# Performance work log

Hardware: AMD Instinct MI355X
Metric: run time of the kernel (lower is better)

## Reference

```python
import jax, jax.numpy as jnp
import numpy as np

B, S, D, H, VOCAB = 4, 2048, 1024, 2048, 32000
E, K, M = 8, 2, 64  # num_experts, top_k, moe_hidden_dim


def gif_forward(x, W, b, decay=0.9, thr=1.0, slope=4.0):
    # GIF neuron layer: linear synaptic current, leaky membrane integration over
    # the sequence dim, surrogate sigmoid spikes with soft reset.
    cur = jnp.einsum('bsd,dh->bsh', x, W) + b  # [B,S,Dout]
    v0 = jnp.zeros((cur.shape[0], cur.shape[2]), cur.dtype)

    def step(v, c):
        v = decay * v + c
        s = jax.nn.sigmoid(slope * (v - thr))
        return v - s * thr, s

    _, spikes = jax.lax.scan(step, v0, jnp.swapaxes(cur, 0, 1))
    return jnp.swapaxes(spikes, 0, 1)  # [B,S,Dout]


def layer_norm(x, g, b, eps=1e-5):
    mu = jnp.mean(x, -1, keepdims=True)
    var = jnp.var(x, -1, keepdims=True)
    return (x - mu) * jax.lax.rsqrt(var + eps) * g + b


def setup_inputs() -> dict:
    key = jax.random.key(0)
    ks = jax.random.split(key, 12)

    def w(k, shape, fan_in):
        return jax.random.normal(k, shape, jnp.float32) / np.sqrt(fan_in).astype(np.float32)

    return {
        'inputs_embeds': jax.random.normal(ks[0], (B, S, D), jnp.float32),
        'input_ids': jax.random.randint(ks[1], (B, S), 0, VOCAB),
        'prosody_table': 0.1 * jax.random.normal(ks[2], (VOCAB,), jnp.float32),
        'enc_W': w(ks[3], (D, H), D), 'enc_b': jnp.zeros((H,), jnp.float32),
        's2c_W': w(ks[4], (H, M), H), 's2c_b': jnp.zeros((M,), jnp.float32),
        'r_W1': w(ks[5], (M, 64), M), 'r_b1': jnp.zeros((64,), jnp.float32),
        'r_W2': w(ks[6], (64, E), 64), 'r_b2': jnp.zeros((E,), jnp.float32),
        'e_W1': w(ks[7], (E, M, H // 2), M), 'e_b1': jnp.zeros((E, H // 2), jnp.float32),
        'e_W2': w(ks[8], (E, H // 2, M), H // 2), 'e_b2': jnp.zeros((E, M), jnp.float32),
        'c2s_W': w(ks[9], (M, H), M), 'c2s_b': jnp.zeros((H,), jnp.float32),
        'dec_W': w(ks[10], (H, D), H), 'dec_b': jnp.zeros((D,), jnp.float32),
        'ln_g': jnp.ones((D,), jnp.float32), 'ln_b': jnp.zeros((D,), jnp.float32),
    }


def reference(inputs_embeds, input_ids, prosody_table, enc_W, enc_b, s2c_W, s2c_b,
              r_W1, r_b1, r_W2, r_b2, e_W1, e_b1, e_W2, e_b2, c2s_W, c2s_b,
              dec_W, dec_b, ln_g, ln_b):
    b, s, d = inputs_embeds.shape
    # Prosody attention bridge: per-token scalar gain from token ids.
    gains = 1.0 + jnp.tanh(prosody_table[input_ids])  # [B,S]
    x = inputs_embeds * gains[..., None]
    spikes = gif_forward(x, enc_W, enc_b)  # [B,S,H]
    # Spike-to-continuous (rate encoding over the singleton time dim) -> [N,M]
    cont = spikes.reshape(b * s, -1) @ s2c_W + s2c_b
    # Liquid MoE router, logits modulated by flattened attention gains.
    logits = (jnp.tanh(cont @ r_W1 + r_b1) @ r_W2 + r_b2) * gains.reshape(-1, 1)
    probs = jax.nn.softmax(logits, axis=-1)  # [N,E]
    topw, topi = jax.lax.top_k(probs, K)
    topw = topw / jnp.sum(topw, axis=-1, keepdims=True)
    # combine[n,e] = sum_k topw[n,k] * [topi[n,k]==e]  (masked-accumulation weights)
    combine = jnp.sum(topw[..., None] * jax.nn.one_hot(topi, E, dtype=probs.dtype), axis=1)
    # Dense-for-all-experts, faithful to the original masked loop.
    h = jax.nn.relu(jnp.einsum('nm,emh->enh', cont, e_W1) + e_b1[:, None, :])  # [E,N,H/2]
    ex_out = jnp.einsum('enh,ehm->enm', h, e_W2) + e_b2[:, None, :]  # [E,N,M]
    moe = jnp.einsum('enm,ne->nm', ex_out, combine)  # [N,M]
    # Continuous-to-spike poisson bridge: T identical rate copies; mean over the
    # copy dim (view(B,S,-1,H).mean(dim=2)) collapses back to the rate itself.
    rates = jax.nn.sigmoid(moe @ c2s_W + c2s_b)  # [N,H]
    spikes_avg = rates.reshape(b, s, -1) * gains[..., None]
    decoded = gif_forward(spikes_avg, dec_W, dec_b)  # [B,S,D]
    return layer_norm(decoded, ln_g, ln_b)
```

## Files before the change

### kernel.cpp

```cpp
#include <hip/hip_runtime.h>
#include <math.h>

#define B_ 4
#define S_ 2048
#define D_ 1024
#define H_ 2048
#define N_TOK 8192
#define HALO 256
#define VOCAB_ 32000

typedef short bf16x8 __attribute__((ext_vector_type(8)));
typedef float f32x4 __attribute__((ext_vector_type(4)));

__device__ __forceinline__ float sigf(float x) {
  return 1.0f / (1.0f + __expf(-x));
}
__device__ __forceinline__ float bf2f(unsigned short u) {
  union { unsigned int i; float f; } x; x.i = ((unsigned int)u) << 16; return x.f;
}
__device__ __forceinline__ unsigned short f2bf(float f) {
  union { float f; unsigned int i; } x; x.f = f;
  unsigned int r = x.i + 0x7fffu + ((x.i >> 16) & 1u);
  return (unsigned short)(r >> 16);
}

__global__ __launch_bounds__(256) void k_gains(const int* __restrict__ ids,
    const float* __restrict__ table, float* __restrict__ gains) {
  int i = blockIdx.x*256 + threadIdx.x;
  int id = ids[i];
  id = id < 0 ? 0 : (id >= VOCAB_ ? VOCAB_-1 : id);
  gains[i] = 1.0f + tanhf(table[id]);
}

__global__ __launch_bounds__(256) void k_genc(
    const float* __restrict__ A, int lda,
    const float* __restrict__ W, int ldw, int c0,
    const float* __restrict__ bias,
    const float* __restrict__ gains,
    float* __restrict__ C, int ldc,
    int K, int mode)
{
  __shared__ float As2[16][132];
  __shared__ float Bs[16][128];
  const int tid = threadIdx.x;
  const int tx = tid & 15;
  const int ty = tid >> 4;
  const int bm = blockIdx.y * 128;
  const int bn = blockIdx.x * 128;

  double acc[8][8];
  float part[8][8];
  #pragma unroll
  for (int i = 0; i < 8; ++i)
    #pragma unroll
    for (int j = 0; j < 8; ++j) { acc[i][j] = 0.0; part[i][j] = 0.f; }

  const int e = tid * 8;
  const int ar = e >> 4, ak = e & 15;
  const int bk = e >> 7, bc = e & 127;

  for (int k0 = 0; k0 < K; k0 += 16) {
    {
      const float* pa = A + (size_t)(bm + ar)*lda + k0 + ak;
      float4 v0 = *(const float4*)pa;
      float4 v1 = *(const float4*)(pa + 4);
      As2[ak+0][ar] = v0.x; As2[ak+1][ar] = v0.y;
      As2[ak+2][ar] = v0.z; As2[ak+3][ar] = v0.w;
      As2[ak+4][ar] = v1.x; As2[ak+5][ar] = v1.y;
      As2[ak+6][ar] = v1.z; As2[ak+7][ar] = v1.w;
    }
    {
      const float* pw = W + (size_t)(k0 + bk)*ldw + c0 + bn + bc;
      *(float4*)&Bs[bk][bc]   = *(const float4*)pw;
      *(float4*)&Bs[bk][bc+4] = *(const float4*)(pw + 4);
    }
    __syncthreads();
    #pragma unroll
    for (int kk = 0; kk < 16; ++kk) {
      float a8[8], b8[8];
      *(float4*)&a8[0] = *(const float4*)&As2[kk][ty*8];
      *(float4*)&a8[4] = *(const float4*)&As2[kk][ty*8+4];
      *(float4*)&b8[0] = *(const float4*)&Bs[kk][tx*8];
      *(float4*)&b8[4] = *(const float4*)&Bs[kk][tx*8+4];
      #pragma unroll
      for (int i = 0; i < 8; ++i)
        #pragma unroll
        for (int j = 0; j < 8; ++j)
          part[i][j] += a8[i]*b8[j];
    }
    __syncthreads();
    #pragma unroll
    for (int i = 0; i < 8; ++i)
      #pragma unroll
      for (int j = 0; j < 8; ++j) { acc[i][j] += (double)part[i][j]; part[i][j] = 0.f; }
  }

  #pragma unroll
  for (int i = 0; i < 8; ++i) {
    const int row = bm + ty*8 + i;
    const double g = (mode >= 2) ? (double)gains[row] : 0.0;
    #pragma unroll
    for (int j = 0; j < 8; ++j) {
      const int col = bn + tx*8 + j;
      const size_t idx = (size_t)row*ldc + col;
      if (mode == 0)      C[idx] = (float)acc[i][j];
      else if (mode == 1) C[idx] += (float)acc[i][j];
      else if (mode == 2) C[idx] = (float)(g*((double)C[idx] + acc[i][j]) + (double)bias[c0+col]);
      else                C[idx] = (float)(g*acc[i][j] + (double)bias[c0+col]);
    }
  }
}

__global__ __launch_bounds__(256) void k_splitT(const float* __restrict__ in,
    unsigned short* __restrict__ outh, unsigned short* __restrict__ outl) {
  __shared__ unsigned short th[32][33];
  __shared__ unsigned short tl[32][33];
  int c0 = blockIdx.x*32, r0 = blockIdx.y*32;
  int tx = threadIdx.x & 31, ty = threadIdx.x >> 5;
  #pragma unroll
  for (int i = 0; i < 32; i += 8) {
    float x = in[(size_t)(r0+ty+i)*H_ + (c0+tx)];
    unsigned short h = f2bf(x);
    th[ty+i][tx] = h;
    tl[ty+i][tx] = f2bf(x - bf2f(h));
  }
  __syncthreads();
  #pragma unroll
  for (int i = 0; i < 32; i += 8) {
    outh[(size_t)(c0+ty+i)*D_ + (r0+tx)] = th[tx][ty+i];
    outl[(size_t)(c0+ty+i)*D_ + (r0+tx)] = tl[tx][ty+i];
  }
}

__global__ __launch_bounds__(256) void k_tsplit(const float* __restrict__ in,
    unsigned short* __restrict__ oh, unsigned short* __restrict__ ol,
    int R, int C) {
  __shared__ unsigned short th[32][33];
  __shared__ unsigned short tl[32][33];
  const size_t mat = (size_t)R*C;
  in += (size_t)blockIdx.z * mat;
  oh += (size_t)blockIdx.z * mat;
  ol += (size_t)blockIdx.z * mat;
  int c0 = blockIdx.x*32, r0 = blockIdx.y*32;
  int tx = threadIdx.x & 31, ty = threadIdx.x >> 5;
  #pragma unroll
  for (int i = 0; i < 32; i += 8) {
    float x = in[(size_t)(r0+ty+i)*C + (c0+tx)];
    unsigned short h = f2bf(x);
    th[ty+i][tx] = h;
    tl[ty+i][tx] = f2bf(x - bf2f(h));
  }
  __syncthreads();
  #pragma unroll
  for (int i = 0; i < 32; i += 8) {
    oh[(size_t)(c0+ty+i)*R + (r0+tx)] = th[tx][ty+i];
    ol[(size_t)(c0+ty+i)*R + (r0+tx)] = tl[tx][ty+i];
  }
}

__global__ __launch_bounds__(256) void k_asplit(const float* __restrict__ in,
    unsigned short* __restrict__ oh, unsigned short* __restrict__ ol) {
  const size_t i = ((size_t)blockIdx.x*256 + threadIdx.x) * 8;
  float4 v0 = *(const float4*)(in + i);
  float4 v1 = *(const float4*)(in + i + 4);
  float xs[8] = {v0.x, v0.y, v0.z, v0.w, v1.x, v1.y, v1.z, v1.w};
  unsigned int hp[4], lp[4];
  #pragma unroll
  for (int t = 0; t < 4; ++t) {
    unsigned short h0 = f2bf(xs[2*t]);
    unsigned short h1 = f2bf(xs[2*t+1]);
    unsigned short l0 = f2bf(xs[2*t]   - bf2f(h0));
    unsigned short l1 = f2bf(xs[2*t+1] - bf2f(h1));
    hp[t] = (unsigned)h0 | ((unsigned)h1 << 16);
    lp[t] = (unsigned)l0 | ((unsigned)l1 << 16);
  }
  *(uint4*)(oh + i) = make_uint4(hp[0], hp[1], hp[2], hp[3]);
  *(uint4*)(ol + i) = make_uint4(lp[0], lp[1], lp[2], lp[3]);
}

__global__ __launch_bounds__(256) void k_egemm(
    const float* __restrict__ A,
    const unsigned short* __restrict__ Bh,
    const unsigned short* __restrict__ Bl,
    const float* __restrict__ bias,
    const float* __restrict__ gains,
    float* __restrict__ C)
{
  __shared__ __align__(16) unsigned short Ahs[128*40];
  __shared__ __align__(16) unsigned short Als[128*40];
  __shared__ __align__(16) unsigned short Bhs[128*40];
  __shared__ __align__(16) unsigned short Bls[128*40];
  const int tid  = threadIdx.x;
  const int lane = tid & 63;
  const int wave = tid >> 6;
  const int wm = (wave >> 1) * 64;
  const int wn = (wave & 1) * 64;
  const int bm = blockIdx.y * 128;
  const int bn = blockIdx.x * 128;
  const int fml = lane & 15;
  const int q  = lane >> 4;
  const int r0a  = tid >> 2;
  const int sseg = tid & 3;

  f32x4 acc[4][4] = {};

  for (int k0 = 0; k0 < 1024; k0 += 32) {
    #pragma unroll
    for (int half = 0; half < 2; ++half) {
      int r = r0a + half*64;
      const float* pa = A + (size_t)(bm + r)*1024 + k0 + sseg*8;
      float4 v0 = *(const float4*)pa;
      float4 v1 = *(const float4*)(pa + 4);
      float xs[8] = {v0.x, v0.y, v0.z, v0.w, v1.x, v1.y, v1.z, v1.w};
      unsigned int hp[4], lp[4];
      #pragma unroll
      for (int t = 0; t < 4; ++t) {
        unsigned short h0 = f2bf(xs[2*t]);
        unsigned short h1 = f2bf(xs[2*t+1]);
        unsigned short l0 = f2bf(xs[2*t]   - bf2f(h0));
        unsigned short l1 = f2bf(xs[2*t+1] - bf2f(h1));
        hp[t] = (unsigned)h0 | ((unsigned)h1 << 16);
        lp[t] = (unsigned)l0 | ((unsigned)l1 << 16);
      }
      *(uint4*)(&Ahs[r*40 + sseg*8]) = make_uint4(hp[0], hp[1], hp[2], hp[3]);
      *(uint4*)(&Als[r*40 + sseg*8]) = make_uint4(lp[0], lp[1], lp[2], lp[3]);
      *(uint4*)(&Bhs[r*40 + sseg*8]) = *(const uint4*)(Bh + (size_t)(bn + r)*1024 + k0 + sseg*8);
      *(uint4*)(&Bls[r*40 + sseg*8]) = *(const uint4*)(Bl + (size_t)(bn + r)*1024 + k0 + sseg*8);
    }
    __syncthreads();
    bf16x8 afh[4], afl[4], bfh[4], bfl[4];
    #pragma unroll
    for (int i = 0; i < 4; ++i) {
      afh[i] = *(const bf16x8*)(&Ahs[(wm + i*16 + fml)*40 + q*8]);
      afl[i] = *(const bf16x8*)(&Als[(wm + i*16 + fml)*40 + q*8]);
    }
    #pragma unroll
    for (int j = 0; j < 4; ++j) {
      bfh[j] = *(const bf16x8*)(&Bhs[(wn + j*16 + fml)*40 + q*8]);
      bfl[j] = *(const bf16x8*)(&Bls[(wn + j*16 + fml)*40 + q*8]);
    }
    #pragma unroll
    for (int i = 0; i < 4; ++i)
      #pragma unroll
      for (int j = 0; j < 4; ++j) {
        acc[i][j] = __builtin_amdgcn_mfma_f32_16x16x32_bf16(afl[i], bfh[j], acc[i][j], 0, 0, 0);
        acc[i][j] = __builtin_amdgcn_mfma_f32_16x16x32_bf16(afh[i], bfl[j], acc[i][j], 0, 0, 0);
        acc[i][j] = __builtin_amdgcn_mfma_f32_16x16x32_bf16(afh[i], bfh[j], acc[i][j], 0, 0, 0);
      }
    __syncthreads();
  }
  #pragma unroll
  for (int i = 0; i < 4; ++i) {
    #pragma unroll
    for (int j = 0; j < 4; ++j) {
      int col = bn + wn + j*16 + fml;
      float bv = bias[col];
      #pragma unroll
      for (int r = 0; r < 4; ++r) {
        int row = bm + wm + i*16 + q*4 + r;
        C[(size_t)row*D_ + col] = gains[row]*acc[i][j][r] + bv;
      }
    }
  }
}

__global__ __launch_bounds__(256) void k_egemm3(
    const unsigned short* __restrict__ Ah, const unsigned short* __restrict__ Al,
    const unsigned short* __restrict__ Bh, const unsigned short* __restrict__ Bl,
    const float* __restrict__ bias,
    const float* __restrict__ gains,
    float* __restrict__ C)
{
  __shared__ __align__(16) unsigned short Ahs[128*40];
  __shared__ __align__(16) unsigned short Als[128*40];
  __shared__ __align__(16) unsigned short Bhs[128*40];
  __shared__ __align__(16) unsigned short Bls[128*40];
  const int tid  = threadIdx.x;
  const int lane = tid & 63;
  const int wave = tid >> 6;
  const int wm = (wave >> 1) * 64;
  const int wn = (wave & 1) * 64;
  const int flat = blockIdx.y * 8 + blockIdx.x;
  const int swz  = (flat & 7) * 64 + (flat >> 3);
  const int bn = (swz & 7) * 128;
  const int bm = (swz >> 3) * 128;
  const int fml = lane & 15;
  const int q  = lane >> 4;
  const int r0a  = tid >> 2;
  const int sseg = tid & 3;

  f32x4 acc[4][4] = {};

  for (int k0 = 0; k0 < 1024; k0 += 32) {
    #pragma unroll
    for (int half = 0; half < 2; ++half) {
      int r = r0a + half*64;
      *(uint4*)(&Ahs[r*40 + sseg*8]) = *(const uint4*)(Ah + (size_t)(bm + r)*1024 + k0 + sseg*8);
      *(uint4*)(&Als[r*40 + sseg*8]) = *(const uint4*)(Al + (size_t)(bm + r)*1024 + k0 + sseg*8);
      *(uint4*)(&Bhs[r*40 + sseg*8]) = *(const uint4*)(Bh + (size_t)(bn + r)*1024 + k0 + sseg*8);
      *(uint4*)(&Bls[r*40 + sseg*8]) = *(const uint4*)(Bl + (size_t)(bn + r)*1024 + k0 + sseg*8);
    }
    __syncthreads();
    bf16x8 afh[4], afl[4], bfh[4], bfl[4];
    #pragma unroll
    for (int i = 0; i < 4; ++i) {
      afh[i] = *(const bf16x8*)(&Ahs[(wm + i*16 + fml)*40 + q*8]);
      afl[i] = *(const bf16x8*)(&Als[(wm + i*16 + fml)*40 + q*8]);
    }
    #pragma unroll
    for (int j = 0; j < 4; ++j) {
      bfh[j] = *(const bf16x8*)(&Bhs[(wn + j*16 + fml)*40 + q*8]);
      bfl[j] = *(const bf16x8*)(&Bls[(wn + j*16 + fml)*40 + q*8]);
    }
    #pragma unroll
    for (int i = 0; i < 4; ++i)
      #pragma unroll
      for (int j = 0; j < 4; ++j) {
        acc[i][j] = __builtin_amdgcn_mfma_f32_16x16x32_bf16(afl[i], bfh[j], acc[i][j], 0, 0, 0);
        acc[i][j] = __builtin_amdgcn_mfma_f32_16x16x32_bf16(afh[i], bfl[j], acc[i][j], 0, 0, 0);
        acc[i][j] = __builtin_amdgcn_mfma_f32_16x16x32_bf16(afh[i], bfh[j], acc[i][j], 0, 0, 0);
      }
    __syncthreads();
  }
  #pragma unroll
  for (int i = 0; i < 4; ++i) {
    #pragma unroll
    for (int j = 0; j < 4; ++j) {
      int col = bn + wn + j*16 + fml;
      float bv = bias[col];
      #pragma unroll
      for (int r = 0; r < 4; ++r) {
        int row = bm + wm + i*16 + q*4 + r;
        C[(size_t)row*D_ + col] = gains[row]*acc[i][j][r] + bv;
      }
    }
  }
}

__global__ __launch_bounds__(256) void k_gif_warm32(const float* __restrict__ buf,
    float* __restrict__ vinit, int Wd, int CS, int Stot)
{
  int c = blockIdx.x*256 + threadIdx.x;
  int channels = gridDim.x*256;
  int chunk = blockIdx.y;
  int b = c / Wd, h = c - b*Wd;
  int s_emit = chunk*CS;
  int s0 = s_emit - HALO; if (s0 < 0) s0 = 0;
  const float* p = buf + (size_t)b*Stot*Wd + h;
  float v = 0.f;
  for (int sg = s0; sg < s_emit; sg += 8) {
    float cv[8];
    #pragma unroll
    for (int i = 0; i < 8; ++i) cv[i] = p[(size_t)(sg+i)*Wd];
    #pragma unroll
    for (int i = 0; i < 8; ++i) {
      v = 0.9f*v + cv[i];
      float s = 1.0f/(1.0f + __expf(-4.0f*(v - 1.0f)));
      v -= s;
    }
  }
  vinit[(size_t)chunk*channels + c] = v;
}

__global__ __launch_bounds__(256) void k_gif_emit32(float* __restrict__ buf,
    const float* __restrict__ vinit, int Wd, int CS, int Stot)
{
  int c = blockIdx.x*256 + threadIdx.x;
  int channels = gridDim.x*256;
  int chunk = blockIdx.y;
  int b = c / Wd, h = c - b*Wd;
  float* p = buf + (size_t)b*Stot*Wd + h + (size_t)chunk*CS*Wd;
  float v = vinit[(size_t)chunk*channels + c];
  float cv[8], nv[8] = {0,0,0,0,0,0,0,0};
  #pragma unroll
  for (int i = 0; i < 8; ++i) cv[i] = p[(size_t)i*Wd];
  for (int sg = 0; sg < CS; sg += 8) {
    float sp[8];
    #pragma unroll
    for (int i = 0; i < 8; ++i) {
      v = 0.9f*v + cv[i];
      float s = 1.0f/(1.0f + __expf(-4.0f*(v - 1.0f)));
      v -= s; sp[i] = s;
    }
    if (sg + 8 < CS) {
      #pragma unroll
      for (int i = 0; i < 8; ++i) nv[i] = p[(size_t)(sg+8+i)*Wd];
    }
    #pragma unroll
    for (int i = 0; i < 8; ++i) p[(size_t)(sg+i)*Wd] = sp[i];
    #pragma unroll
    for (int i = 0; i < 8; ++i) cv[i] = nv[i];
  }
}

__global__ __launch_bounds__(256) void k_s2c(const float* __restrict__ Sp, int ldS, int KH,
    const float* __restrict__ W, size_t woff, float* __restrict__ out, int accum,
    const float* __restrict__ bias2) {
  __shared__ float As_[16][17];
  __shared__ float Ws_[16][68];
  const int bm = blockIdx.x * 16;
  const int tid = threadIdx.x;
  const int rt = tid >> 4;
  const int ct = tid & 15;
  float acc[4] = {};
  for (int k0 = 0; k0 < KH; k0 += 16) {
    As_[tid >> 4][tid & 15] = Sp[(size_t)(bm + (tid >> 4))*ldS + k0 + (tid & 15)];
    #pragma unroll
    for (int i = 0; i < 4; ++i) {
      int e = tid + i*256;
      Ws_[e >> 6][e & 63] = W[woff + (size_t)(k0 + (e >> 6))*64 + (e & 63)];
    }
    __syncthreads();
    #pragma unroll
    for (int kk = 0; kk < 16; ++kk) {
      float a = As_[rt][kk];
      #pragma unroll
      for (int j = 0; j < 4; ++j) acc[j] += a * Ws_[kk][ct*4+j];
    }
    __syncthreads();
  }
  #pragma unroll
  for (int j = 0; j < 4; ++j) {
    size_t idx = ((size_t)bm + rt)*64 + ct*4 + j;
    float a = acc[j];
    if (accum) {
      float v = out[idx] + a;
      if (bias2) v = v + bias2[ct*4+j];
      out[idx] = v;
    } else out[idx] = a;
  }
}

__global__ void k_zero(int* p) { if (threadIdx.x < 8) p[threadIdx.x] = 0; }

__global__ __launch_bounds__(256) void k_rhid(const float* __restrict__ cont,
    const float* __restrict__ rW1, const float* __restrict__ rb1,
    float* __restrict__ hidden)
{
  __shared__ float W1s[64*64];
  __shared__ float cs[16][64];
  const int tid = threadIdx.x;
  const int j  = tid & 63;
  const int tg = tid >> 6;
  const int n0 = blockIdx.x * 16;
  for (int i = tid; i < 64*64; i += 256) W1s[i] = rW1[i];
  #pragma unroll
  for (int i = 0; i < 4; ++i) {
    int e = tid + i*256;
    cs[e >> 6][e & 63] = cont[(size_t)(n0 + (e >> 6))*64 + (e & 63)];
  }
  __syncthreads();
  const float b1 = rb1[j];
  float t0 = b1, t1 = b1, t2 = b1, t3 = b1;
  #pragma unroll
  for (int m = 0; m < 64; ++m) {
    const float w = W1s[m*64 + j];
    t0 += cs[tg*4+0][m] * w;
    t1 += cs[tg*4+1][m] * w;
    t2 += cs[tg*4+2][m] * w;
    t3 += cs[tg*4+3][m] * w;
  }
  const size_t base = (size_t)(n0 + tg*4)*64 + j;
  hidden[base]       = tanhf(t0);
  hidden[base + 64]  = tanhf(t1);
  hidden[base + 128] = tanhf(t2);
  hidden[base + 192] = tanhf(t3);
}

__global__ __launch_bounds__(64) void k_rtop(const float* __restrict__ hidden,
    const float* __restrict__ rW2, const float* __restrict__ rb2,
    const float* __restrict__ gains,
    int* __restrict__ cnt, unsigned int* __restrict__ list, float* __restrict__ lw)
{
  __shared__ float W2s[64*8];
  __shared__ float b2s[8];
  __shared__ int bcnt[8];
  __shared__ int bbase[8];
  const int tid = threadIdx.x;
  const int n = blockIdx.x*64 + tid;
  for (int i = tid; i < 64*8; i += 64) W2s[i] = rW2[i];
  if (tid < 8) { b2s[tid] = rb2[tid]; bcnt[tid] = 0; }
  __syncthreads();
  float lg[8];
  #pragma unroll
  for (int e = 0; e < 8; ++e) lg[e] = b2s[e];
  const float* hp = hidden + (size_t)n*64;
  #pragma unroll 8
  for (int j = 0; j < 64; ++j) {
    float t = hp[j];
    #pragma unroll
    for (int e = 0; e < 8; ++e) lg[e] += t * W2s[j*8 + e];
  }
  float g = gains[n];
  #pragma unroll
  for (int e = 0; e < 8; ++e) lg[e] *= g;
  int i1 = 0; float m1 = lg[0];
  #pragma unroll
  for (int e = 1; e < 8; ++e) if (lg[e] > m1) { m1 = lg[e]; i1 = e; }
  int i2 = (i1 == 0) ? 1 : 0; float m2 = lg[i2];
  #pragma unroll
  for (int e = 0; e < 8; ++e) if (e != i1 && lg[e] > m2) { m2 = lg[e]; i2 = e; }
  float w1 = 1.0f / (1.0f + __expf(m2 - m1));
  int p1l = atomicAdd(&bcnt[i1], 1);
  int p2l = atomicAdd(&bcnt[i2], 1);
  __syncthreads();
  if (tid < 8) bbase[tid] = bcnt[tid] ? atomicAdd(&cnt[tid], bcnt[tid]) : 0;
  __syncthreads();
  const int p1 = bbase[i1] + p1l;
  list[i1*8192 + p1] = ((unsigned)n << 1);
  lw[i1*8192 + p1] = w1;
  const int p2 = bbase[i2] + p2l;
  list[i2*8192 + p2] = ((unsigned)n << 1) | 1u;
  lw[i2*8192 + p2] = 1.0f - w1;
}

__global__ __launch_bounds__(256) void k_expgrp(
    const float* __restrict__ cont,
    const unsigned int* __restrict__ list, const float* __restrict__ lw,
    const int* __restrict__ cnt,
    const float* __restrict__ eW1, const float* __restrict__ eb1,
    const float* __restrict__ eW2, const float* __restrict__ eb2,
    float* __restrict__ eout)
{
  const int e = blockIdx.y;
  const int t0 = blockIdx.x * 64;
  const int ce = cnt[e];
  if (t0 >= ce) return;
  const int nt = (ce - t0 < 64) ? (ce - t0) : 64;
  __shared__ float ct[64][65];
  __shared__ float w1b[64][65];
  __shared__ float hbl[64][65];
  __shared__ float w2b[64][65];
  __shared__ unsigned int sl[64];
  __shared__ float swt[64];
  const int tid = threadIdx.x;
  if (tid < 64) {
    if (tid < nt) {
      sl[tid]  = list[e*8192 + t0 + tid];
      swt[tid] = lw[e*8192 + t0 + tid];
    } else { sl[tid] = 0; swt[tid] = 0.f; }
  }
  __syncthreads();
  for (int f = tid; f < 64*64; f += 256) {
    int r = f >> 6, m = f & 63;
    ct[r][m] = (r < nt) ? cont[(size_t)(sl[r] >> 1)*64 + m] : 0.f;
  }
  const float* W1 = eW1 + (size_t)e*64*1024;
  const float* W2 = eW2 + (size_t)e*1024*64;
  const float* B1 = eb1 + (size_t)e*1024;
  const int rt = tid >> 4, c16 = tid & 15;
  float outa[4][4] = {};
  for (int hc = 0; hc < 1024; hc += 64) {
    __syncthreads();
    for (int f = tid; f < 64*64; f += 256) {
      int m = f >> 6, j = f & 63;
      w1b[m][j] = W1[(size_t)m*1024 + hc + j];
      w2b[m][j] = W2[(size_t)(hc + m)*64 + j];
    }
    __syncthreads();
    float h4[4][4];
    #pragma unroll
    for (int i = 0; i < 4; ++i) {
      #pragma unroll
      for (int j = 0; j < 4; ++j) h4[i][j] = B1[hc + c16*4 + j];
    }
    #pragma unroll 16
    for (int m = 0; m < 64; ++m) {
      float a4[4], b4[4];
      #pragma unroll
      for (int i = 0; i < 4; ++i) a4[i] = ct[rt*4+i][m];
      #pragma unroll
      for (int j = 0; j < 4; ++j) b4[j] = w1b[m][c16*4+j];
      #pragma unroll
      for (int i = 0; i < 4; ++i)
        #pragma unroll
        for (int j = 0; j < 4; ++j) h4[i][j] += a4[i]*b4[j];
    }
    #pragma unroll
    for (int i = 0; i < 4; ++i)
      #pragma unroll
      for (int j = 0; j < 4; ++j)
        hbl[rt*4+i][c16*4+j] = fmaxf(h4[i][j], 0.f);
    __syncthreads();
    #pragma unroll 16
    for (int j = 0; j < 64; ++j) {
      float a4[4], b4[4];
      #pragma unroll
      for (int i = 0; i < 4; ++i) a4[i] = hbl[rt*4+i][j];
      #pragma unroll
      for (int nn = 0; nn < 4; ++nn) b4[nn] = w2b[j][c16*4+nn];
      #pragma unroll
      for (int i = 0; i < 4; ++i)
        #pragma unroll
        for (int nn = 0; nn < 4; ++nn) outa[i][nn] += a4[i]*b4[nn];
    }
  }
  #pragma unroll
  for (int i = 0; i < 4; ++i) {
    int r = rt*4 + i;
    if (r < nt) {
      float w = swt[r];
      #pragma unroll
      for (int nn = 0; nn < 4; ++nn) {
        int col = c16*4 + nn;
        eout[(size_t)sl[r]*64 + col] = w * (outa[i][nn] + eb2[(size_t)e*64 + col]);
      }
    }
  }
}

__global__ __launch_bounds__(256) void k_expmfma(
    const float* __restrict__ cont,
    const unsigned int* __restrict__ list, const float* __restrict__ lw,
    const int* __restrict__ cnt,
    const unsigned short* __restrict__ w1h, const unsigned short* __restrict__ w1l,
    const float* __restrict__ eb1,
    const unsigned short* __restrict__ w2h, const unsigned short* __restrict__ w2l,
    const float* __restrict__ eb2,
    float* __restrict__ eout)
{
  const int e  = blockIdx.y;
  const int t0 = blockIdx.x * 64;
  const int ce = cnt[e];
  if (t0 >= ce) return;
  const int nt = (ce - t0 < 64) ? (ce - t0) : 64;

  __shared__ __align__(16) unsigned short cth[64*72],  ctl[64*72];
  __shared__ __align__(16) unsigned short w1sh[64*72], w1sl[64*72];
  __shared__ __align__(16) unsigned short w2sh[64*72], w2sl[64*72];
  __shared__ __align__(16) unsigned short hsh[64*72],  hsl[64*72];
  __shared__ unsigned int sl[64];
  __shared__ float swt[64];

  const int tid  = threadIdx.x;
  const int lane = tid & 63;
  const int wave = tid >> 6;
  const int wm  = (wave >> 1) * 32;
  const int wn  = (wave & 1) * 32;
  const int fml = lane & 15;
  const int q   = lane >> 4;

  if (tid < 64) {
    if (tid < nt) { sl[tid] = list[e*8192 + t0 + tid]; swt[tid] = lw[e*8192 + t0 + tid]; }
    else          { sl[tid] = 0; swt[tid] = 0.f; }
  }
  __syncthreads();

  {
    const int row = tid >> 2;
    const int m0  = (tid & 3) * 16;
    float x[16] = {0.f,0.f,0.f,0.f,0.f,0.f,0.f,0.f,0.f,0.f,0.f,0.f,0.f,0.f,0.f,0.f};
    if (row < nt) {
      const float* p = cont + (size_t)(sl[row] >> 1)*64 + m0;
      *(float4*)&x[0]  = *(const float4*)(p);
      *(float4*)&x[4]  = *(const float4*)(p + 4);
      *(float4*)&x[8]  = *(const float4*)(p + 8);
      *(float4*)&x[12] = *(const float4*)(p + 12);
    }
    unsigned int hp[8], lp[8];
    #pragma unroll
    for (int t = 0; t < 8; ++t) {
      unsigned short h0 = f2bf(x[2*t]);
      unsigned short h1 = f2bf(x[2*t+1]);
      unsigned short l0 = f2bf(x[2*t]   - bf2f(h0));
      unsigned short l1 = f2bf(x[2*t+1] - bf2f(h1));
      hp[t] = (unsigned)h0 | ((unsigned)h1 << 16);
      lp[t] = (unsigned)l0 | ((unsigned)l1 << 16);
    }
    *(uint4*)&cth[row*72 + m0]     = make_uint4(hp[0], hp[1], hp[2], hp[3]);
    *(uint4*)&cth[row*72 + m0 + 8] = make_uint4(hp[4], hp[5], hp[6], hp[7]);
    *(uint4*)&ctl[row*72 + m0]     = make_uint4(lp[0], lp[1], lp[2], lp[3]);
    *(uint4*)&ctl[row*72 + m0 + 8] = make_uint4(lp[4], lp[5], lp[6], lp[7]);
  }

  f32x4 acc2[2][2] = {};

  for (int hc = 0; hc < 1024; hc += 64) {
    {
      const int row = tid >> 2;
      const int seg = (tid & 3) * 16;
      const size_t o1 = ((size_t)(e*1024 + hc + row))*64 + seg;
      *(uint4*)&w1sh[row*72 + seg]     = *(const uint4*)(w1h + o1);
      *(uint4*)&w1sh[row*72 + seg + 8] = *(const uint4*)(w1h + o1 + 8);
      *(uint4*)&w1sl[row*72 + seg]     = *(const uint4*)(w1l + o1);
      *(uint4*)&w1sl[row*72 + seg + 8] = *(const uint4*)(w1l + o1 + 8);
      const size_t o2 = ((size_t)(e*64 + row))*1024 + hc + seg;
      *(uint4*)&w2sh[row*72 + seg]     = *(const uint4*)(w2h + o2);
      *(uint4*)&w2sh[row*72 + seg + 8] = *(const uint4*)(w2h + o2 + 8);
      *(uint4*)&w2sl[row*72 + seg]     = *(const uint4*)(w2l + o2);
      *(uint4*)&w2sl[row*72 + seg + 8] = *(const uint4*)(w2l + o2 + 8);
    }
    __syncthreads();

    f32x4 acc1[2][2] = {};
    #pragma unroll
    for (int ks = 0; ks < 2; ++ks) {
      bf16x8 ah[2], al[2], bh[2], bl[2];
      #pragma unroll
      for (int i = 0; i < 2; ++i) {
        ah[i] = *(const bf16x8*)&cth[(wm + i*16 + fml)*72 + ks*32 + q*8];
        al[i] = *(const bf16x8*)&ctl[(wm + i*16 + fml)*72 + ks*32 + q*8];
      }
      #pragma unroll
      for (int j = 0; j < 2; ++j) {
        bh[j] = *(const bf16x8*)&w1sh[(wn + j*16 + fml)*72 + ks*32 + q*8];
        bl[j] = *(const bf16x8*)&w1sl[(wn + j*16 + fml)*72 + ks*32 + q*8];
      }
      #pragma unroll
      for (int i = 0; i < 2; ++i)
        #pragma unroll
        for (int j = 0; j < 2; ++j) {
          acc1[i][j] = __builtin_amdgcn_mfma_f32_16x16x32_bf16(al[i], bh[j], acc1[i][j], 0, 0, 0);
          acc1[i][j] = __builtin_amdgcn_mfma_f32_16x16x32_bf16(ah[i], bl[j], acc1[i][j], 0, 0, 0);
          acc1[i][j] = __builtin_amdgcn_mfma_f32_16x16x32_bf16(ah[i], bh[j], acc1[i][j], 0, 0, 0);
        }
    }

    #pragma unroll
    for (int j = 0; j < 2; ++j) {
      const int col = wn + j*16 + fml;
      const float b1 = eb1[(size_t)e*1024 + hc + col];
      #pragma unroll
      for (int i = 0; i < 2; ++i) {
        #pragma unroll
        for (int r = 0; r < 4; ++r) {
          const int trow = wm + i*16 + q*4 + r;
          float v = fmaxf(acc1[i][j][r] + b1, 0.f);
          unsigned short hh = f2bf(v);
          hsh[trow*72 + col] = hh;
          hsl[trow*72 + col] = f2bf(v - bf2f(hh));
        }
      }
    }
    __syncthreads();

    #pragma unroll
    for (int ks = 0; ks < 2; ++ks) {
      bf16x8 ah[2], al[2], bh[2], bl[2];
      #pragma unroll
      for (int i = 0; i < 2; ++i) {
        ah[i] = *(const bf16x8*)&hsh[(wm + i*16 + fml)*72 + ks*32 + q*8];
        al[i] = *(const bf16x8*)&hsl[(wm + i*16 + fml)*72 + ks*32 + q*8];
      }
      #pragma unroll
      for (int j = 0; j < 2; ++j) {
        bh[j] = *(const bf16x8*)&w2sh[(wn + j*16 + fml)*72 + ks*32 + q*8];
        bl[j] = *(const bf16x8*)&w2sl[(wn + j*16 + fml)*72 + ks*32 + q*8];
      }
      #pragma unroll
      for (int i = 0; i < 2; ++i)
        #pragma unroll
        for (int j = 0; j < 2; ++j) {
          acc2[i][j] = __builtin_amdgcn_mfma_f32_16x16x32_bf16(al[i], bh[j], acc2[i][j], 0, 0, 0);
          acc2[i][j] = __builtin_amdgcn_mfma_f32_16x16x32_bf16(ah[i], bl[j], acc2[i][j], 0, 0, 0);
          acc2[i][j] = __builtin_amdgcn_mfma_f32_16x16x32_bf16(ah[i], bh[j], acc2[i][j], 0, 0, 0);
        }
    }
    __syncthreads();
  }

  #pragma unroll
  for (int j = 0; j < 2; ++j) {
    const int col = wn + j*16 + fml;
    const float b2 = eb2[(size_t)e*64 + col];
    #pragma unroll
    for (int i = 0; i < 2; ++i) {
      #pragma unroll
      for (int r = 0; r < 4; ++r) {
        const int trow = wm + i*16 + q*4 + r;
        if (trow < nt)
          eout[(size_t)sl[trow]*64 + col] = swt[trow]*(acc2[i][j][r] + b2);
      }
    }
  }
}

__global__ __launch_bounds__(256) void k_c2sM(
    const float* __restrict__ eoutTok,
    const unsigned short* __restrict__ WTh,
    const unsigned short* __restrict__ WTl,
    const float* __restrict__ bias,
    unsigned short* __restrict__ rates)
{
  __shared__ __align__(16) unsigned short Ahs[128*72], Als[128*72];
  __shared__ __align__(16) unsigned short Bhs[128*72], Bls[128*72];
  const int tid  = threadIdx.x;
  const int lane = tid & 63;
  const int wave = tid >> 6;
  const int wm = (wave >> 1) * 64;
  const int wn = (wave & 1) * 64;
  const int bm = blockIdx.y * 128;
  const int bn = blockIdx.x * 128;
  const int fml = lane & 15;
  const int q  = lane >> 4;

  {
    const int row = tid >> 1;
    const int m0  = (tid & 1) * 32;
    const float* p = eoutTok + (size_t)(bm + row)*128 + m0;
    float x[32];
    #pragma unroll
    for (int i = 0; i < 8; ++i) {
      float4 a = *(const float4*)(p + i*4);
      float4 b = *(const float4*)(p + 64 + i*4);
      x[i*4+0] = a.x + b.x; x[i*4+1] = a.y + b.y;
      x[i*4+2] = a.z + b.z; x[i*4+3] = a.w + b.w;
    }
    unsigned int hp[16], lp[16];
    #pragma unroll
    for (int t = 0; t < 16; ++t) {
      unsigned short h0 = f2bf(x[2*t]);
      unsigned short h1 = f2bf(x[2*t+1]);
      unsigned short l0 = f2bf(x[2*t]   - bf2f(h0));
      unsigned short l1 = f2bf(x[2*t+1] - bf2f(h1));
      hp[t] = (unsigned)h0 | ((unsigned)h1 << 16);
      lp[t] = (unsigned)l0 | ((unsigned)l1 << 16);
    }
    #pragma unroll
    for (int t = 0; t < 4; ++t) {
      *(uint4*)&Ahs[row*72 + m0 + t*8] = make_uint4(hp[t*4+0],hp[t*4+1],hp[t*4+2],hp[t*4+3]);
      *(uint4*)&Als[row*72 + m0 + t*8] = make_uint4(lp[t*4+0],lp[t*4+1],lp[t*4+2],lp[t*4+3]);
    }
    const unsigned short* ph = WTh + (size_t)(bn + row)*64 + m0;
    const unsigned short* pl = WTl + (size_t)(bn + row)*64 + m0;
    #pragma unroll
    for (int t = 0; t < 4; ++t) {
      *(uint4*)&Bhs[row*72 + m0 + t*8] = *(const uint4*)(ph + t*8);
      *(uint4*)&Bls[row*72 + m0 + t*8] = *(const uint4*)(pl + t*8);
    }
  }
  __syncthreads();

  f32x4 acc[4][4] = {};
  #pragma unroll
  for (int ks = 0; ks < 2; ++ks) {
    bf16x8 ah[4], al[4], bh[4], bl[4];
    #pragma unroll
    for (int i = 0; i < 4; ++i) {
      ah[i] = *(const bf16x8*)&Ahs[(wm + i*16 + fml)*72 + ks*32 + q*8];
      al[i] = *(const bf16x8*)&Als[(wm + i*16 + fml)*72 + ks*32 + q*8];
    }
    #pragma unroll
    for (int j = 0; j < 4; ++j) {
      bh[j] = *(const bf16x8*)&Bhs[(wn + j*16 + fml)*72 + ks*32 + q*8];
      bl[j] = *(const bf16x8*)&Bls[(wn + j*16 + fml)*72 + ks*32 + q*8];
    }
    #pragma unroll
    for (int i = 0; i < 4; ++i)
      #pragma unroll
      for (int j = 0; j < 4; ++j) {
        acc[i][j] = __builtin_amdgcn_mfma_f32_16x16x32_bf16(al[i], bh[j], acc[i][j], 0, 0, 0);
        acc[i][j] = __builtin_amdgcn_mfma_f32_16x16x32_bf16(ah[i], bl[j], acc[i][j], 0, 0, 0);
        acc[i][j] = __builtin_amdgcn_mfma_f32_16x16x32_bf16(ah[i], bh[j], acc[i][j], 0, 0, 0);
      }
  }

  #pragma unroll
  for (int j = 0; j < 4; ++j) {
    const int col = bn + wn + j*16 + fml;
    const float bv = bias[col];
    #pragma unroll
    for (int i = 0; i < 4; ++i) {
      #pragma unroll
      for (int r = 0; r < 4; ++r) {
        const int row = bm + wm + i*16 + q*4 + r;
        rates[(size_t)row*H_ + col] = f2bf(sigf(acc[i][j][r] + bv));
      }
    }
  }
}

__global__ __launch_bounds__(256) void k_c2sS(const float* __restrict__ eoutTok,
    const float* __restrict__ W, int coff,
    const float* __restrict__ bias, float* __restrict__ rat)
{
  __shared__ float ml[8][64];
  const int tid = threadIdx.x;
  const int n0 = blockIdx.x * 8;
  for (int i = tid; i < 512; i += 256) {
    int t = i >> 6, m = i & 63;
    ml[t][m] = eoutTok[(size_t)(n0+t)*128 + m] + eoutTok[(size_t)(n0+t)*128 + 64 + m];
  }
  __syncthreads();
  float acc[8] = {};
  for (int m = 0; m < 64; ++m) {
    float wv = W[(size_t)m*H_ + coff + tid];
    #pragma unroll
    for (int t = 0; t < 8; ++t) acc[t] += ml[t][m] * wv;
  }
  float bv = bias[coff + tid];
  #pragma unroll
  for (int t = 0; t < 8; ++t)
    rat[(size_t)(n0+t)*256 + tid] = sigf(acc[t] + bv);
}

__global__ __launch_bounds__(256) void k_transb(const float* __restrict__ in,
    unsigned short* __restrict__ out, int R, int C) {
  __shared__ unsigned short t[32][33];
  int c0 = blockIdx.x*32, r0 = blockIdx.y*32;
  int tx = threadIdx.x & 31, ty = threadIdx.x >> 5;
  #pragma unroll
  for (int i = 0; i < 32; i += 8)
    t[ty+i][tx] = f2bf(in[(size_t)(r0+ty+i)*C + (c0+tx)]);
  __syncthreads();
  #pragma unroll
  for (int i = 0; i < 32; i += 8)
    out[(size_t)(c0+ty+i)*R + (r0+tx)] = t[tx][ty+i];
}

__global__ __launch_bounds__(256) void k_dgemm(
    const unsigned short* __restrict__ A,
    const unsigned short* __restrict__ BT,
    const float* __restrict__ bias,
    const float* __restrict__ gains,
    float* __restrict__ C)
{
  __shared__ __align__(16) unsigned short As[128*40];
  __shared__ __align__(16) unsigned short Bs[128*40];
  const int tid  = threadIdx.x;
  const int lane = tid & 63;
  const int wave = tid >> 6;
  const int wm = (wave >> 1) * 64;
  const int wn = (wave & 1) * 64;
  const int bm = blockIdx.y * 128;
  const int bn = blockIdx.x * 128;
  const int fml = lane & 15;
  const int q  = lane >> 4;
  const int r0a  = tid >> 2;
  const int sseg = tid & 3;

  f32x4 acc[4][4] = {};

  for (int k0 = 0; k0 < H_; k0 += 32) {
    #pragma unroll
    for (int half = 0; half < 2; ++half) {
      int r = r0a + half*64;
      *(uint4*)(&As[r*40 + sseg*8]) = *(const uint4*)(A + (size_t)(bm + r)*H_ + k0 + sseg*8);
      *(uint4*)(&Bs[r*40 + sseg*8]) = *(const uint4*)(BT + (size_t)(bn + r)*H_ + k0 + sseg*8);
    }
    __syncthreads();
    bf16x8 af[4], bfr[4];
    #pragma unroll
    for (int i = 0; i < 4; ++i)
      af[i] = *(const bf16x8*)(&As[(wm + i*16 + fml)*40 + q*8]);
    #pragma unroll
    for (int j = 0; j < 4; ++j)
      bfr[j] = *(const bf16x8*)(&Bs[(wn + j*16 + fml)*40 + q*8]);
    #pragma unroll
    for (int i = 0; i < 4; ++i)
      #pragma unroll
      for (int j = 0; j < 4; ++j)
        acc[i][j] = __builtin_amdgcn_mfma_f32_16x16x32_bf16(af[i], bfr[j], acc[i][j], 0, 0, 0);
    __syncthreads();
  }
  #pragma unroll
  for (int i = 0; i < 4; ++i) {
    #pragma unroll
    for (int j = 0; j < 4; ++j) {
      int col = bn + wn + j*16 + fml;
      float bv = bias[col];
      #pragma unroll
      for (int r = 0; r < 4; ++r) {
        int row = bm + wm + i*16 + q*4 + r;
        C[(size_t)row*D_ + col] = gains[row]*acc[i][j][r] + bv;
      }
    }
  }
}

__global__ __launch_bounds__(256) void k_ln(float* __restrict__ X,
    const float* __restrict__ g, const float* __restrict__ b)
{
  const int n = blockIdx.x, tid = threadIdx.x;
  float4* row = (float4*)(X + (size_t)n*D_);
  const float4 xv = row[tid];
  float xa[4] = {xv.x, xv.y, xv.z, xv.w};
  float s = xa[0]+xa[1]+xa[2]+xa[3];
  float ss = xa[0]*xa[0]+xa[1]*xa[1]+xa[2]*xa[2]+xa[3]*xa[3];
  #pragma unroll
  for (int off = 32; off >= 1; off >>= 1) {
    s  += __shfl_down(s, off);
    ss += __shfl_down(ss, off);
  }
  __shared__ float rs[4], rss[4];
  const int lane = tid & 63, wv = tid >> 6;
  if (lane == 0) { rs[wv] = s; rss[wv] = ss; }
  __syncthreads();
  float S0 = rs[0]+rs[1]+rs[2]+rs[3];
  float SS = rss[0]+rss[1]+rss[2]+rss[3];
  float mu = S0 * (1.f/(float)D_);
  float var = SS * (1.f/(float)D_) - mu*mu;
  float inv = rsqrtf(var + 1e-5f);
  int idx = tid*4;
  float4 o;
  o.x = (xa[0]-mu)*inv*g[idx+0] + b[idx+0];
  o.y = (xa[1]-mu)*inv*g[idx+1] + b[idx+1];
  o.z = (xa[2]-mu)*inv*g[idx+2] + b[idx+2];
  o.w = (xa[3]-mu)*inv*g[idx+3] + b[idx+3];
  row[tid] = o;
}

extern "C" void kernel_launch(void* const* d_in, const int* in_sizes, int n_in,
                              void* d_out, int out_size, void* d_ws, size_t ws_size,
                              hipStream_t stream) {
  (void)in_sizes; (void)n_in; (void)out_size;
  const float* embeds = (const float*)d_in[0];
  const int*   ids    = (const int*)d_in[1];
  const float* pros   = (const float*)d_in[2];
  const float* enc_W  = (const float*)d_in[3];
  const float* enc_b  = (const float*)d_in[4];
  const float* s2c_W  = (const float*)d_in[5];
  const float* s2c_b  = (const float*)d_in[6];
  const float* r_W1   = (const float*)d_in[7];
  const float* r_b1   = (const float*)d_in[8];
  const float* r_W2   = (const float*)d_in[9];
  const float* r_b2   = (const float*)d_in[10];
  const float* e_W1   = (const float*)d_in[11];
  const float* e_b1   = (const float*)d_in[12];
  const float* e_W2   = (const float*)d_in[13];
  const float* e_b2   = (const float*)d_in[14];
  const float* c2s_W  = (const float*)d_in[15];
  const float* c2s_b  = (const float*)d_in[16];
  const float* dec_W  = (const float*)d_in[17];
  const float* dec_b  = (const float*)d_in[18];
  const float* ln_g   = (const float*)d_in[19];
  const float* ln_b   = (const float*)d_in[20];

  char* ws = (char*)d_ws;
  float*          contp = (float*)ws;
  unsigned short* c2sWTh= (unsigned short*)(ws + (size_t)0x200000);
  unsigned short* c2sWTl= (unsigned short*)(ws + (size_t)0x280000);
  float*          eout  = (float*)(ws + (size_t)0x400000);
  float*          hidden= (float*)(ws + (size_t)0x400000);
  float*          gains = (float*)(ws + (size_t)0x800000);
  int*            cnt   = (int*)(ws + (size_t)0x808000);
  unsigned int*   list  = (unsigned int*)(ws + (size_t)0x809000);
  float*          lw    = (float*)(ws + (size_t)0x849000);
  float*          vinitF= (float*)(ws + (size_t)0x890000);
  unsigned short* WhT   = (unsigned short*)(ws + (size_t)0x900000);
  unsigned short* WlT   = (unsigned short*)(ws + (size_t)0xD00000);
  unsigned short* encAh = (unsigned short*)(ws + (size_t)0x1100000);
  unsigned short* encAl = (unsigned short*)(ws + (size_t)0x2100000);
  unsigned short* decWT = WhT;
  unsigned short* rates = WlT;
  float*          ratSf = (float*)ws;
  float*          cur   = (float*)d_out;

  unsigned short* w1th = WhT;
  unsigned short* w1tl = w1th + (size_t)8*1024*64;
  unsigned short* w2th = w1tl + (size_t)8*1024*64;
  unsigned short* w2tl = w2th + (size_t)8*1024*64;

  const int encM  = (ws_size >= (size_t)18*1024*1024) ? 1 : 0;
  const int encPA = (encM && ws_size >= (size_t)50*1024*1024) ? 1 : 0;
  const int T = (ws_size >= (size_t)46*1024*1024) ? 8192
              : (ws_size >= (size_t)30*1024*1024) ? 4096 : 0;

  k_gains<<<N_TOK/256, 256, 0, stream>>>(ids, pros, gains);
  k_zero<<<1, 64, 0, stream>>>(cnt);

  if (encM) {
    k_splitT<<<dim3(64, 32), 256, 0, stream>>>(enc_W, WhT, WlT);
    if (encPA)
      k_asplit<<<4096, 256, 0, stream>>>(embeds, encAh, encAl);
    for (int c = 0; c < 2; ++c) {
      if (encPA) {
        k_egemm3<<<dim3(8, 64), 256, 0, stream>>>(
            encAh, encAl, WhT + (size_t)c*1024*1024, WlT + (size_t)c*1024*1024,
            enc_b + c*1024, gains, cur);
      } else {
        k_egemm<<<dim3(8, 64), 256, 0, stream>>>(
            embeds, WhT + (size_t)c*1024*1024, WlT + (size_t)c*1024*1024,
            enc_b + c*1024, gains, cur);
      }
      k_gif_warm32<<<dim3(16, 16), 256, 0, stream>>>(cur, vinitF, 1024, 128, S_);
      k_gif_emit32<<<dim3(16, 16), 256, 0, stream>>>(cur, vinitF, 1024, 128, S_);
      k_s2c<<<N_TOK/16, 256, 0, stream>>>(cur, 1024, 1024,
          s2c_W, (size_t)c*1024*64, contp, (c > 0),
          (c == 1) ? s2c_b : (const float*)nullptr);
    }
    k_tsplit<<<dim3(32, 2, 8), 256, 0, stream>>>(e_W1, w1th, w1tl, 64, 1024);
    k_tsplit<<<dim3(2, 32, 8), 256, 0, stream>>>(e_W2, w2th, w2tl, 1024, 64);
  } else {
    for (int c = 0; c < 2; ++c) {
      k_genc<<<dim3(8, 64), 256, 0, stream>>>(
          embeds, D_, enc_W, H_, c*1024, enc_b, gains, cur, 1024, D_, 3);
      k_gif_warm32<<<dim3(16, 16), 256, 0, stream>>>(cur, vinitF, 1024, 128, S_);
      k_gif_emit32<<<dim3(16, 16), 256, 0, stream>>>(cur, vinitF, 1024, 128, S_);
      k_s2c<<<N_TOK/16, 256, 0, stream>>>(cur, 1024, 1024,
          s2c_W, (size_t)c*1024*64, contp, (c > 0),
          (c == 1) ? s2c_b : (const float*)nullptr);
    }
  }

  k_rhid<<<N_TOK/16, 256, 0, stream>>>(contp, r_W1, r_b1, hidden);
  k_rtop<<<N_TOK/64, 64, 0, stream>>>(hidden, r_W2, r_b2, gains, cnt, list, lw);

  if (encM) {
    k_expmfma<<<dim3(128, 8), 256, 0, stream>>>(contp, list, lw, cnt,
        w1th, w1tl, e_b1, w2th, w2tl, e_b2, eout);
  } else {
    k_expgrp<<<dim3(128, 8), 256, 0, stream>>>(contp, list, lw, cnt,
        e_W1, e_b1, e_W2, e_b2, eout);
  }

  if (T > 0) {
    k_transb<<<dim3(32, 64), 256, 0, stream>>>(dec_W, decWT, H_, D_);
    k_tsplit<<<dim3(64, 2, 1), 256, 0, stream>>>(c2s_W, c2sWTh, c2sWTl, 64, H_);
    for (int tok0 = 0; tok0 < N_TOK; tok0 += T) {
      k_c2sM<<<dim3(H_/128, T/128), 256, 0, stream>>>(eout + (size_t)tok0*128,
          c2sWTh, c2sWTl, c2s_b, rates);
      float* cur2 = (float*)d_out + (size_t)tok0*D_;
      k_dgemm<<<dim3(D_/128, T/128), 256, 0, stream>>>(
          rates, decWT, dec_b, gains + tok0, cur2);
      int channels = (T/2048)*1024;
      k_gif_warm32<<<dim3(channels/256, 8), 256, 0, stream>>>(cur2, vinitF, D_, 256, S_);
      k_gif_emit32<<<dim3(channels/256, 8), 256, 0, stream>>>(cur2, vinitF, D_, 256, S_);
      k_ln<<<T, 256, 0, stream>>>(cur2, ln_g, ln_b);
    }
  } else {
    for (int hb = 0; hb < 2; ++hb) {
      float* cur2 = (float*)d_out + (size_t)hb*4096*D_;
      for (int kh = 0; kh < 8; ++kh) {
        k_c2sS<<<4096/8, 256, 0, stream>>>(eout + (size_t)hb*4096*128,
            c2s_W, kh*256, c2s_b, ratSf);
        int mode = (kh == 0) ? 0 : ((kh < 7) ? 1 : 2);
        k_genc<<<dim3(8, 32), 256, 0, stream>>>(
            ratSf, 256, dec_W + (size_t)kh*256*D_, D_, 0, dec_b,
            gains + hb*4096, cur2, D_, 256, mode);
      }
      k_gif_warm32<<<dim3(8, 8), 256, 0, stream>>>(cur2, vinitF, D_, 256, S_);
      k_gif_emit32<<<dim3(8, 8), 256, 0, stream>>>(cur2, vinitF, D_, 256, S_);
      k_ln<<<4096, 256, 0, stream>>>(cur2, ln_g, ln_b);
    }
  }
}
```

Baseline: 659.8 us.

## Fuse router hidden and top-k kernels, swizzle dgemm and expert grid order

Merges the router's tanh hidden-layer kernel and its top-2 selection kernel into one kernel that keeps the hidden activations in shared memory. This removes one launch and a global write and read of the hidden buffer. Separately, the expert MFMA grid is transposed so the expert index varies fastest, and the decoder GEMM remaps block indices with a swizzle meant to improve L2 reuse. The fused router does its top-k on only 16 threads per block, which leaves most lanes idle in that phase.

```diff
diff --git a/kernel.cpp b/kernel.cpp
--- a/kernel.cpp
+++ b/kernel.cpp
@@ -433,85 +433,87 @@
 
 __global__ void k_zero(int* p) { if (threadIdx.x < 8) p[threadIdx.x] = 0; }
 
-__global__ __launch_bounds__(256) void k_rhid(const float* __restrict__ cont,
+__global__ __launch_bounds__(256) void k_router2(const float* __restrict__ cont,
     const float* __restrict__ rW1, const float* __restrict__ rb1,
-    float* __restrict__ hidden)
+    const float* __restrict__ rW2, const float* __restrict__ rb2,
+    const float* __restrict__ gains,
+    int* __restrict__ cnt, unsigned int* __restrict__ list, float* __restrict__ lw)
 {
   __shared__ float W1s[64*64];
+  __shared__ float W2s[64*8];
+  __shared__ float b2s[8];
   __shared__ float cs[16][64];
+  __shared__ float hs[16][65];
+  __shared__ int bcnt[8];
+  __shared__ int bbase[8];
   const int tid = threadIdx.x;
   const int j  = tid & 63;
   const int tg = tid >> 6;
   const int n0 = blockIdx.x * 16;
   for (int i = tid; i < 64*64; i += 256) W1s[i] = rW1[i];
+  for (int i = tid; i < 64*8; i += 256)  W2s[i] = rW2[i];
+  if (tid < 8) { b2s[tid] = rb2[tid]; bcnt[tid] = 0; }
   #pragma unroll
   for (int i = 0; i < 4; ++i) {
     int e = tid + i*256;
     cs[e >> 6][e & 63] = cont[(size_t)(n0 + (e >> 6))*64 + (e & 63)];
   }
   __syncthreads();
-  const float b1 = rb1[j];
-  float t0 = b1, t1 = b1, t2 = b1, t3 = b1;
-  #pragma unroll
-  for (int m = 0; m < 64; ++m) {
-    const float w = W1s[m*64 + j];
-    t0 += cs[tg*4+0][m] * w;
-    t1 += cs[tg*4+1][m] * w;
-    t2 += cs[tg*4+2][m] * w;
-    t3 += cs[tg*4+3][m] * w;
-  }
-  const size_t base = (size_t)(n0 + tg*4)*64 + j;
-  hidden[base]       = tanhf(t0);
-  hidden[base + 64]  = tanhf(t1);
-  hidden[base + 128] = tanhf(t2);
-  hidden[base + 192] = tanhf(t3);
-}
-
-__global__ __launch_bounds__(64) void k_rtop(const float* __restrict__ hidden,
-    const float* __restrict__ rW2, const float* __restrict__ rb2,
-    const float* __restrict__ gains,
-    int* __restrict__ cnt, unsigned int* __restrict__ list, float* __restrict__ lw)
-{
-  __shared__ float W2s[64*8];
-  __shared__ float b2s[8];
-  __shared__ int bcnt[8];
-  __shared__ int bbase[8];
-  const int tid = threadIdx.x;
-  const int n = blockIdx.x*64 + tid;
-  for (int i = tid; i < 64*8; i += 64) W2s[i] = rW2[i];
-  if (tid < 8) { b2s[tid] = rb2[tid]; bcnt[tid] = 0; }
+  {
+    const float b1 = rb1[j];
+    float t0 = b1, t1 = b1, t2 = b1, t3 = b1;
+    #pragma unroll
+    for (int m = 0; m < 64; ++m) {
+      const float w = W1s[m*64 + j];
+      t0 += cs[tg*4+0][m] * w;
+      t1 += cs[tg*4+1][m] * w;
+      t2 += cs[tg*4+2][m] * w;
+      t3 += cs[tg*4+3][m] * w;
+    }
+    hs[tg*4+0][j] = tanhf(t0);
+    hs[tg*4+1][j] = tanhf(t1);
+    hs[tg*4+2][j] = tanhf(t2);
+    hs[tg*4+3][j] = tanhf(t3);
+  }
   __syncthreads();
-  float lg[8];
-  #pragma unroll
-  for (int e = 0; e < 8; ++e) lg[e] = b2s[e];
-  const float* hp = hidden + (size_t)n*64;
-  #pragma unroll 8
-  for (int j = 0; j < 64; ++j) {
-    float t = hp[j];
-    #pragma unroll
-    for (int e = 0; e < 8; ++e) lg[e] += t * W2s[j*8 + e];
-  }
-  float g = gains[n];
-  #pragma unroll
-  for (int e = 0; e < 8; ++e) lg[e] *= g;
-  int i1 = 0; float m1 = lg[0];
-  #pragma unroll
-  for (int e = 1; e < 8; ++e) if (lg[e] > m1) { m1 = lg[e]; i1 = e; }
-  int i2 = (i1 == 0) ? 1 : 0; float m2 = lg[i2];
-  #pragma unroll
-  for (int e = 0; e < 8; ++e) if (e != i1 && lg[e] > m2) { m2 = lg[e]; i2 = e; }
-  float w1 = 1.0f / (1.0f + __expf(m2 - m1));
-  int p1l = atomicAdd(&bcnt[i1], 1);
-  int p2l = atomicAdd(&bcnt[i2], 1);
+  int i1 = 0, i2 = 0, p1l = 0, p2l = 0;
+  float w1 = 0.f;
+  if (tid < 16) {
+    const int n = n0 + tid;
+    float lg[8];
+    #pragma unroll
+    for (int e = 0; e < 8; ++e) lg[e] = b2s[e];
+    #pragma unroll 8
+    for (int jj = 0; jj < 64; ++jj) {
+      float t = hs[tid][jj];
+      #pragma unroll
+      for (int e = 0; e < 8; ++e) lg[e] += t * W2s[jj*8 + e];
+    }
+    float g = gains[n];
+    #pragma unroll
+    for (int e = 0; e < 8; ++e) lg[e] *= g;
+    float m1 = lg[0];
+    #pragma unroll
+    for (int e = 1; e < 8; ++e) if (lg[e] > m1) { m1 = lg[e]; i1 = e; }
+    i2 = (i1 == 0) ? 1 : 0; float m2 = lg[i2];
+    #pragma unroll
+    for (int e = 0; e < 8; ++e) if (e != i1 && lg[e] > m2) { m2 = lg[e]; i2 = e; }
+    w1 = 1.0f / (1.0f + __expf(m2 - m1));
+    p1l = atomicAdd(&bcnt[i1], 1);
+    p2l = atomicAdd(&bcnt[i2], 1);
+  }
   __syncthreads();
   if (tid < 8) bbase[tid] = bcnt[tid] ? atomicAdd(&cnt[tid], bcnt[tid]) : 0;
   __syncthreads();
-  const int p1 = bbase[i1] + p1l;
-  list[i1*8192 + p1] = ((unsigned)n << 1);
-  lw[i1*8192 + p1] = w1;
-  const int p2 = bbase[i2] + p2l;
-  list[i2*8192 + p2] = ((unsigned)n << 1) | 1u;
-  lw[i2*8192 + p2] = 1.0f - w1;
+  if (tid < 16) {
+    const int n = n0 + tid;
+    const int p1 = bbase[i1] + p1l;
+    list[i1*8192 + p1] = ((unsigned)n << 1);
+    lw[i1*8192 + p1] = w1;
+    const int p2 = bbase[i2] + p2l;
+    list[i2*8192 + p2] = ((unsigned)n << 1) | 1u;
+    lw[i2*8192 + p2] = 1.0f - w1;
+  }
 }
 
 __global__ __launch_bounds__(256) void k_expgrp(
@@ -619,8 +621,8 @@
     const float* __restrict__ eb2,
     float* __restrict__ eout)
 {
-  const int e  = blockIdx.y;
-  const int t0 = blockIdx.x * 64;
+  const int e  = blockIdx.x;
+  const int t0 = blockIdx.y * 64;
   const int ce = cnt[e];
   if (t0 >= ce) return;
   const int nt = (ce - t0 < 64) ? (ce - t0) : 64;
@@ -922,8 +924,11 @@
   const int wave = tid >> 6;
   const int wm = (wave >> 1) * 64;
   const int wn = (wave & 1) * 64;
-  const int bm = blockIdx.y * 128;
-  const int bn = blockIdx.x * 128;
+  const int gy   = gridDim.y;
+  const int flat = blockIdx.y * 8 + blockIdx.x;
+  const int swz  = (flat & 7) * gy + (flat >> 3);
+  const int bn = (swz & 7) * 128;
+  const int bm = (swz >> 3) * 128;
   const int fml = lane & 15;
   const int q  = lane >> 4;
   const int r0a  = tid >> 2;
@@ -1031,7 +1036,6 @@
   unsigned short* c2sWTh= (unsigned short*)(ws + (size_t)0x200000);
   unsigned short* c2sWTl= (unsigned short*)(ws + (size_t)0x280000);
   float*          eout  = (float*)(ws + (size_t)0x400000);
-  float*          hidden= (float*)(ws + (size_t)0x400000);
   float*          gains = (float*)(ws + (size_t)0x800000);
   int*            cnt   = (int*)(ws + (size_t)0x808000);
   unsigned int*   list  = (unsigned int*)(ws + (size_t)0x809000);
@@ -1093,11 +1097,11 @@
     }
   }
 
-  k_rhid<<<N_TOK/16, 256, 0, stream>>>(contp, r_W1, r_b1, hidden);
-  k_rtop<<<N_TOK/64, 64, 0, stream>>>(hidden, r_W2, r_b2, gains, cnt, list, lw);
+  k_router2<<<N_TOK/16, 256, 0, stream>>>(contp, r_W1, r_b1, r_W2, r_b2,
+                                          gains, cnt, list, lw);
 
   if (encM) {
-    k_expmfma<<<dim3(128, 8), 256, 0, stream>>>(contp, list, lw, cnt,
+    k_expmfma<<<dim3(8, 128), 256, 0, stream>>>(contp, list, lw, cnt,
         w1th, w1tl, e_b1, w2th, w2tl, e_b2, eout);
   } else {
     k_expgrp<<<dim3(128, 8), 256, 0, stream>>>(contp, list, lw, cnt,
```

Measured after the change: 677.2 us. 1.03x slower.
